# Optimization experiments

Hardware: AMD Instinct MI355X
Metric: run time of the kernel (lower is better)

Reference implementation:

```python
import jax, jax.numpy as jnp
import numpy as np

RADIUS = 0.1
NSAMPLE = 32
B, N, NPOINT, C = 2, 16384, 4096, 64


def setup_inputs() -> dict:
    key = jax.random.key(0)
    k1, k2, k3 = jax.random.split(key, 3)
    xyz = jax.random.uniform(k1, (B, N, 3), dtype=jnp.float32)
    new_xyz = jax.random.uniform(k2, (B, NPOINT, 3), dtype=jnp.float32)
    features = jax.random.normal(k3, (B, C, N), dtype=jnp.float32)
    return {"xyz": xyz, "new_xyz": new_xyz, "features": features}


def ball_query(radius, nsample, xyz, new_xyz):
    # xyz: (B, N, 3), new_xyz: (B, npoint, 3) -> idx: (B, npoint, nsample) int32
    # Semantics of the CUDA ball_query: take the first `nsample` points (in
    # original order) whose squared distance < radius^2; pad remaining slots
    # with the first in-ball index (0 if the ball is empty).
    d2 = jnp.sum((new_xyz[:, :, None, :] - xyz[:, None, :, :]) ** 2, axis=-1)  # (B, npoint, N)
    mask = d2 < radius * radius
    # stable argsort puts in-ball indices first, preserving original order
    order = jnp.argsort(jnp.where(mask, 0, 1), axis=-1)  # (B, npoint, N)
    cnt = jnp.sum(mask, axis=-1, keepdims=True)  # (B, npoint, 1)
    first = jnp.where(cnt > 0, order[..., :1], 0)  # (B, npoint, 1)
    slots = jnp.arange(nsample)
    idx = jnp.where(slots < cnt, order[..., :nsample], first)
    return idx.astype(jnp.int32)


def group(features, idx):
    # features: (B, C, N), idx: (B, npoint, nsample) -> (B, C, npoint, nsample)
    return jax.vmap(lambda f, i: f[:, i])(features, idx)


def reference(xyz, new_xyz, features):
    idx = ball_query(RADIUS, NSAMPLE, xyz, new_xyz)  # (B, npoint, nsample)
    xyz_t = jnp.transpose(xyz, (0, 2, 1))  # (B, 3, N)
    grouped_xyz = group(xyz_t, idx)  # (B, 3, npoint, nsample)
    grouped_xyz = grouped_xyz - jnp.transpose(new_xyz, (0, 2, 1))[..., None]
    grouped_features = group(features, idx)  # (B, C, npoint, nsample)
    new_features = jnp.concatenate([grouped_xyz, grouped_features], axis=1)
    return new_features  # (B, 3 + C, npoint, nsample)
```

## Files before the change

### kernel.cpp

```cpp
#include <hip/hip_runtime.h>

#define B 2
#define N 16384
#define NPOINT 4096
#define C 64
#define NSAMPLE 32

#define NCELL 1000
#define CELLW_STRIDE 1024
#define OFF_STRIDE 1056
#define CAP 192

__device__ __forceinline__ float r2_thresh() { return (float)(0.1 * 0.1); }

__device__ __forceinline__ int clamp09(int v) { return v < 0 ? 0 : (v > 9 ? 9 : v); }

__device__ __forceinline__ int cell_of(float x, float y, float z) {
    const int ix = clamp09((int)floorf(x * 10.0f));
    const int iy = clamp09((int)floorf(y * 10.0f));
    const int iz = clamp09((int)floorf(z * 10.0f));
    return (ix * 10 + iy) * 10 + iz;
}

__global__ void __launch_bounds__(256) grid_init_kernel(int* __restrict__ work) {
    const int t = blockIdx.x * blockDim.x + threadIdx.x;
    if (t < 2 * B * CELLW_STRIDE) work[t] = 0;
}

__global__ void __launch_bounds__(256) grid_hist_kernel(
    const float* __restrict__ xyz, const float* __restrict__ new_xyz,
    int* __restrict__ cellwork, int* __restrict__ qwork) {
    const int i = blockIdx.x * blockDim.x + threadIdx.x;
    if (i < B * N) {
        const int b = i / N;
        const float x = xyz[(size_t)i * 3 + 0];
        const float y = xyz[(size_t)i * 3 + 1];
        const float z = xyz[(size_t)i * 3 + 2];
        atomicAdd(&cellwork[b * CELLW_STRIDE + cell_of(x, y, z)], 1);
    } else if (i < B * (N + NPOINT)) {
        const int qi = i - B * N;
        const int b = qi / NPOINT;
        const float x = new_xyz[(size_t)qi * 3 + 0];
        const float y = new_xyz[(size_t)qi * 3 + 1];
        const float z = new_xyz[(size_t)qi * 3 + 2];
        atomicAdd(&qwork[b * CELLW_STRIDE + cell_of(x, y, z)], 1);
    }
}

__global__ void __launch_bounds__(1024) grid_scan_kernel(
    int* __restrict__ cellwork, int* __restrict__ qwork, int* __restrict__ off) {
    __shared__ int s[1024];
    const int blk = blockIdx.x;
    const int t = threadIdx.x;
    int* __restrict__ arr = (blk < B) ? (cellwork + blk * CELLW_STRIDE)
                                      : (qwork + (blk - B) * CELLW_STRIDE);
    const int v = (t < NCELL) ? arr[t] : 0;
    s[t] = v;
    __syncthreads();
#pragma unroll
    for (int d = 1; d < 1024; d <<= 1) {
        const int add = (t >= d) ? s[t - d] : 0;
        __syncthreads();
        s[t] += add;
        __syncthreads();
    }
    const int excl = s[t] - v;
    if (blk < B && t <= NCELL) off[blk * OFF_STRIDE + t] = excl;
    if (t < NCELL) arr[t] = excl;
}

__global__ void __launch_bounds__(256) grid_scatter_kernel(
    const float* __restrict__ xyz, const float* __restrict__ new_xyz,
    int* __restrict__ cellwork, int* __restrict__ qwork,
    float4* __restrict__ binned, int* __restrict__ qperm) {
    const int i = blockIdx.x * blockDim.x + threadIdx.x;
    if (i < B * N) {
        const int b = i / N;
        const int p = i - b * N;
        const float x = xyz[(size_t)i * 3 + 0];
        const float y = xyz[(size_t)i * 3 + 1];
        const float z = xyz[(size_t)i * 3 + 2];
        const int c = cell_of(x, y, z);
        const int pos = atomicAdd(&cellwork[b * CELLW_STRIDE + c], 1);
        float4 v;
        v.x = x; v.y = y; v.z = z; v.w = __int_as_float(p);
        binned[(size_t)b * N + pos] = v;
    } else if (i < B * (N + NPOINT)) {
        const int qi = i - B * N;
        const int b = qi / NPOINT;
        const int j = qi - b * NPOINT;
        const float x = new_xyz[(size_t)qi * 3 + 0];
        const float y = new_xyz[(size_t)qi * 3 + 1];
        const float z = new_xyz[(size_t)qi * 3 + 2];
        const int c = cell_of(x, y, z);
        const int pos = atomicAdd(&qwork[b * CELLW_STRIDE + c], 1);
        qperm[b * NPOINT + pos] = j;
    }
}

__device__ void linear_ball_fallback(const float* __restrict__ xb,
                                     float cx, float cy, float cz,
                                     int lane, unsigned long long lanemask_lt,
                                     int* __restrict__ out) {
    const float r2 = r2_thresh();
    int cnt = 0, first_idx = 0;
    for (int base = 0; base < N; base += 64) {
        const int i = base + lane;
        const float x = xb[i * 3 + 0];
        const float y = xb[i * 3 + 1];
        const float z = xb[i * 3 + 2];
        float d2;
        {
#pragma clang fp contract(off)
            float dx = x - cx;
            float dy = y - cy;
            float dz = z - cz;
            d2 = dx * dx + dy * dy + dz * dz;
        }
        const bool in = d2 < r2;
        const unsigned long long m = __ballot(in);
        if (in) {
            const int pos = cnt + __popcll(m & lanemask_lt);
            if (pos < NSAMPLE) out[pos] = i;
        }
        if (cnt == 0 && m != 0ull) first_idx = base + __builtin_ctzll(m);
        cnt += __popcll(m);
        if (cnt >= NSAMPLE) break;
    }
    if (cnt < NSAMPLE) {
        if (cnt == 0) first_idx = 0;
        for (int pos = cnt + lane; pos < NSAMPLE; pos += 64) out[pos] = first_idx;
    }
}

__global__ void __launch_bounds__(256) ball_query_grid_kernel(
    const float4* __restrict__ binned,
    const int* __restrict__ off,
    const float* __restrict__ new_xyz,
    const float* __restrict__ xyz,
    const int* __restrict__ qperm,
    int* __restrict__ idx_out)
{
    __shared__ int cand_s[4][CAP];
    const int lane = threadIdx.x & 63;
    const int wib = threadIdx.x >> 6;
    const int wave = (blockIdx.x * blockDim.x + threadIdx.x) >> 6;
    if (wave >= B * NPOINT) return;
    const int b = wave / NPOINT;
    const int sp = wave - b * NPOINT;
    const int j = qperm[b * NPOINT + sp];

    const float cx = new_xyz[((size_t)b * NPOINT + j) * 3 + 0];
    const float cy = new_xyz[((size_t)b * NPOINT + j) * 3 + 1];
    const float cz = new_xyz[((size_t)b * NPOINT + j) * 3 + 2];

    int* __restrict__ cand = cand_s[wib];
    const float4* __restrict__ bb = binned + (size_t)b * N;
    const int* __restrict__ ob = off + b * OFF_STRIDE;
    int* __restrict__ out = idx_out + ((size_t)b * NPOINT + j) * NSAMPLE;

    const float r2 = r2_thresh();
    const unsigned long long lanemask_lt = (lane == 63) ? 0x7FFFFFFFFFFFFFFFull
                                                        : ((1ull << lane) - 1ull);

    const int lox = max(0, (int)floorf((cx - 0.1001f) * 10.0f));
    const int hix = min(9, (int)floorf((cx + 0.1001f) * 10.0f));
    const int loy = max(0, (int)floorf((cy - 0.1001f) * 10.0f));
    const int hiy = min(9, (int)floorf((cy + 0.1001f) * 10.0f));
    const int loz = max(0, (int)floorf((cz - 0.1001f) * 10.0f));
    const int hiz = min(9, (int)floorf((cz + 0.1001f) * 10.0f));

    int K = 0;
    for (int ix = lox; ix <= hix; ++ix) {
        for (int iy = loy; iy <= hiy; ++iy) {
            const int rowc = (ix * 10 + iy) * 10;
            const int s0 = ob[rowc + loz];
            const int s1 = ob[rowc + hiz + 1];
            for (int cur = s0; cur < s1; cur += 64) {
                const int i = cur + lane;
                const bool valid = (i < s1);
                float4 pv;
                if (valid) pv = bb[i];
                else { pv.x = 1e9f; pv.y = 1e9f; pv.z = 1e9f; pv.w = 0.0f; }
                float d2;
                {
#pragma clang fp contract(off)
                    float dx = pv.x - cx;
                    float dy = pv.y - cy;
                    float dz = pv.z - cz;
                    d2 = dx * dx + dy * dy + dz * dz;
                }
                const bool in = valid && (d2 < r2);
                const unsigned long long m = __ballot(in);
                if (in) {
                    const int pos = K + __popcll(m & lanemask_lt);
                    if (pos < CAP) cand[pos] = __float_as_int(pv.w);
                }
                K += __popcll(m);
            }
        }
    }

    if (K > CAP) {
        linear_ball_fallback(xyz + (size_t)b * N * 3, cx, cy, cz, lane, lanemask_lt, out);
        return;
    }

    const int e0 = (lane < K) ? cand[lane] : 0x7FFFFFFF;
    const int e1 = (64 + lane < K) ? cand[64 + lane] : 0x7FFFFFFF;
    const int e2 = (128 + lane < K) ? cand[128 + lane] : 0x7FFFFFFF;
    int r0 = 0, r1 = 0, r2i = 0;
    if (K <= 64) {
        for (int k = 0; k < K; ++k) { const int v = cand[k]; r0 += (v < e0); }
    } else if (K <= 128) {
        for (int k = 0; k < K; ++k) { const int v = cand[k]; r0 += (v < e0); r1 += (v < e1); }
    } else {
        for (int k = 0; k < K; ++k) {
            const int v = cand[k];
            r0 += (v < e0); r1 += (v < e1); r2i += (v < e2);
        }
    }
    if (lane < K && r0 < NSAMPLE) out[r0] = e0;
    if (64 + lane < K && r1 < NSAMPLE) out[r1] = e1;
    if (128 + lane < K && r2i < NSAMPLE) out[r2i] = e2;

    if (K < NSAMPLE) {
        int mn = min(e0, min(e1, e2));
#pragma unroll
        for (int d = 32; d; d >>= 1) mn = min(mn, __shfl_xor(mn, d));
        const int fill = (K > 0) ? mn : 0;
        for (int pos = K + lane; pos < NSAMPLE; pos += 64) out[pos] = fill;
    }
}

__global__ void __launch_bounds__(256) ball_query_kernel(
    const float* __restrict__ xyz, const float* __restrict__ new_xyz,
    int* __restrict__ idx_out)
{
    const int wave = (blockIdx.x * blockDim.x + threadIdx.x) >> 6;
    const int lane = threadIdx.x & 63;
    if (wave >= B * NPOINT) return;
    const int b = wave / NPOINT;
    const float cx = new_xyz[(size_t)wave * 3 + 0];
    const float cy = new_xyz[(size_t)wave * 3 + 1];
    const float cz = new_xyz[(size_t)wave * 3 + 2];
    const unsigned long long lanemask_lt = (lane == 63) ? 0x7FFFFFFFFFFFFFFFull
                                                        : ((1ull << lane) - 1ull);
    linear_ball_fallback(xyz + (size_t)b * N * 3, cx, cy, cz, lane, lanemask_lt,
                         idx_out + (size_t)wave * NSAMPLE);
}

__global__ void __launch_bounds__(256) transpose_kernel(
    const float* __restrict__ feat, float* __restrict__ ft) {
    __shared__ float tile[64 * 65];
    const int b = blockIdx.y;
    const int n0 = blockIdx.x * 64;
    const int t = threadIdx.x;
    const int l = t & 63;
    const int w = t >> 6;
#pragma unroll
    for (int it = 0; it < 16; ++it) {
        const int c = it * 4 + w;
        tile[c * 65 + l] = feat[((size_t)b * C + c) * N + n0 + l];
    }
    __syncthreads();
#pragma unroll
    for (int it = 0; it < 16; ++it) {
        const int nn = it * 4 + w;
        ft[((size_t)b * N + n0 + nn) * C + l] = tile[l * 65 + nn];
    }
}

__global__ void __launch_bounds__(256) group2_kernel(
    const float* __restrict__ xyz, const float* __restrict__ new_xyz,
    const float* __restrict__ ft, const int* __restrict__ idx_arr,
    const int* __restrict__ qperm, float* __restrict__ out) {
    __shared__ int sidx[64];
    __shared__ float sf[64 * 65];

    const int t = threadIdx.x;
    const int g = blockIdx.x;
    const int nwg = B * NPOINT / 2;
    const int swz = (g & 7) * (nwg / 8) + (g >> 3);
    const int b = swz / (NPOINT / 2);
    const int p = swz - b * (NPOINT / 2);

    const int q0 = qperm[b * NPOINT + 2 * p + 0];
    const int q1 = qperm[b * NPOINT + 2 * p + 1];

    if (t < 64) {
        const int qq = (t < 32) ? q0 : q1;
        sidx[t] = idx_arr[((size_t)b * NPOINT + qq) * NSAMPLE + (t & 31)];
    }
    __syncthreads();

    {
        const int lane16 = t & 15;
        const int pq = t >> 4;
#pragma unroll
        for (int it = 0; it < 4; ++it) {
            const int pp = it * 16 + pq;
            const int id = sidx[pp];
            const float4 v = *(const float4*)(ft + ((size_t)b * N + id) * C + lane16 * 4);
            float* dst = sf + pp * 65 + lane16 * 4;
            dst[0] = v.x; dst[1] = v.y; dst[2] = v.z; dst[3] = v.w;
        }
    }

    const size_t plane = (size_t)NPOINT * NSAMPLE;
    const size_t bbase = (size_t)b * (3 + C) * plane;

    if (t < 64) {
        const int id = sidx[t];
        const int qq = (t < 32) ? q0 : q1;
        const size_t cb = ((size_t)b * NPOINT + qq) * 3;
        const size_t pb = ((size_t)b * N + id) * 3;
        const size_t ob = bbase + (size_t)qq * NSAMPLE + (t & 31);
        {
#pragma clang fp contract(off)
            out[ob + 0 * plane] = xyz[pb + 0] - new_xyz[cb + 0];
            out[ob + 1 * plane] = xyz[pb + 1] - new_xyz[cb + 1];
            out[ob + 2 * plane] = xyz[pb + 2] - new_xyz[cb + 2];
        }
    }
    __syncthreads();

    const int l = t & 63;
    const int w = t >> 6;
    const int qq = (l < 32) ? q0 : q1;
    const size_t rowbase = bbase + (size_t)qq * NSAMPLE + (l & 31);
#pragma unroll
    for (int it = 0; it < 16; ++it) {
        const int c = it * 4 + w;
        out[rowbase + (size_t)(3 + c) * plane] = sf[l * 65 + c];
    }
}

__global__ void __launch_bounds__(256) group_kernel(
    const float* __restrict__ xyz, const float* __restrict__ new_xyz,
    const float* __restrict__ feat, const int* __restrict__ idx_arr,
    float* __restrict__ out) {
    const int t = threadIdx.x;
    const int s = t & 31;
    const int jl = t >> 5;
    const int j = blockIdx.x * 8 + jl;
    const int b = blockIdx.y;

    const int id = idx_arr[((size_t)b * NPOINT + j) * NSAMPLE + s];

    const float px = xyz[((size_t)b * N + id) * 3 + 0] - new_xyz[((size_t)b * NPOINT + j) * 3 + 0];
    const float py = xyz[((size_t)b * N + id) * 3 + 1] - new_xyz[((size_t)b * NPOINT + j) * 3 + 1];
    const float pz = xyz[((size_t)b * N + id) * 3 + 2] - new_xyz[((size_t)b * NPOINT + j) * 3 + 2];

    const size_t plane = (size_t)NPOINT * NSAMPLE;
    const size_t obase = (size_t)b * (3 + C) * plane + (size_t)j * NSAMPLE + s;

    out[obase + 0 * plane] = px;
    out[obase + 1 * plane] = py;
    out[obase + 2 * plane] = pz;

    const float* __restrict__ fb = feat + (size_t)b * C * N;
#pragma unroll 8
    for (int c = 0; c < C; ++c) {
        out[obase + (size_t)(3 + c) * plane] = fb[(size_t)c * N + id];
    }
}

extern "C" void kernel_launch(void* const* d_in, const int* in_sizes, int n_in,
                              void* d_out, int out_size, void* d_ws, size_t ws_size,
                              hipStream_t stream) {
    const float* xyz     = (const float*)d_in[0];
    const float* new_xyz = (const float*)d_in[1];
    const float* feat    = (const float*)d_in[2];
    float* out = (float*)d_out;

    const size_t idx_bytes    = (size_t)B * NPOINT * NSAMPLE * sizeof(int);
    const size_t ft_bytes     = (size_t)B * N * C * sizeof(float);
    const size_t binned_bytes = (size_t)B * N * sizeof(float4);
    const size_t off_bytes    = (size_t)B * OFF_STRIDE * sizeof(int);
    const size_t cellw_bytes  = (size_t)B * CELLW_STRIDE * sizeof(int);
    const size_t qwork_bytes  = (size_t)B * CELLW_STRIDE * sizeof(int);
    const size_t qperm_bytes  = (size_t)B * NPOINT * sizeof(int);

    char* ws = (char*)d_ws;
    size_t o = 0;
    int*    idx_ws   = (int*)(ws + o);    o += idx_bytes;
    float*  ft       = (float*)(ws + o);  o += ft_bytes;
    float4* binned   = (float4*)(ws + o); o += binned_bytes;
    int*    off      = (int*)(ws + o);    o += off_bytes;
    int*    cellwork = (int*)(ws + o);    o += cellw_bytes;
    int*    qwork    = (int*)(ws + o);    o += qwork_bytes;
    int*    qperm    = (int*)(ws + o);    o += qperm_bytes;

    const bool use_grid = (ws_size >= o);

    if (use_grid) {
        transpose_kernel<<<dim3(N / 64, B), 256, 0, stream>>>(feat, ft);
        grid_init_kernel<<<(2 * B * CELLW_STRIDE + 255) / 256, 256, 0, stream>>>(cellwork);
        grid_hist_kernel<<<(B * (N + NPOINT) + 255) / 256, 256, 0, stream>>>(
            xyz, new_xyz, cellwork, qwork);
        grid_scan_kernel<<<2 * B, 1024, 0, stream>>>(cellwork, qwork, off);
        grid_scatter_kernel<<<(B * (N + NPOINT) + 255) / 256, 256, 0, stream>>>(
            xyz, new_xyz, cellwork, qwork, binned, qperm);
        ball_query_grid_kernel<<<(B * NPOINT) / 4, 256, 0, stream>>>(
            binned, off, new_xyz, xyz, qperm, idx_ws);
        group2_kernel<<<B * NPOINT / 2, 256, 0, stream>>>(
            xyz, new_xyz, ft, idx_ws, qperm, out);
    } else {
        ball_query_kernel<<<(B * NPOINT) / 4, 256, 0, stream>>>(xyz, new_xyz, idx_ws);
        dim3 grid2(NPOINT / 8, B);
        group_kernel<<<grid2, 256, 0, stream>>>(xyz, new_xyz, feat, idx_ws, out);
    }
}
```

Baseline: 54.48 us.

## Process two cell-sorted queries per wave sharing candidate scans when windows match

After: 56.65 us. 4.0% more time.

```diff
diff --git a/kernel.cpp b/kernel.cpp
--- a/kernel.cpp
+++ b/kernel.cpp
@@ -101,7 +101,7 @@
 __device__ void linear_ball_fallback(const float* __restrict__ xb,
                                      float cx, float cy, float cz,
                                      int lane, unsigned long long lanemask_lt,
-                                     int* __restrict__ out) {
+                                     int* out) {
     const float r2 = r2_thresh();
     int cnt = 0, first_idx = 0;
     for (int base = 0; base < N; base += 64) {
@@ -133,43 +133,42 @@
     }
 }
 
-__global__ void __launch_bounds__(256) ball_query_grid_kernel(
-    const float4* __restrict__ binned,
-    const int* __restrict__ off,
-    const float* __restrict__ new_xyz,
-    const float* __restrict__ xyz,
-    const int* __restrict__ qperm,
-    int* __restrict__ idx_out)
+__device__ __forceinline__ void rank_select(const int* cand, int K, int lane,
+                                            int* __restrict__ out) {
+    const int e0 = (lane < K) ? cand[lane] : 0x7FFFFFFF;
+    const int e1 = (64 + lane < K) ? cand[64 + lane] : 0x7FFFFFFF;
+    const int e2 = (128 + lane < K) ? cand[128 + lane] : 0x7FFFFFFF;
+    int r0 = 0, r1 = 0, r2i = 0;
+    if (K <= 64) {
+        for (int k = 0; k < K; ++k) { const int v = cand[k]; r0 += (v < e0); }
+    } else if (K <= 128) {
+        for (int k = 0; k < K; ++k) { const int v = cand[k]; r0 += (v < e0); r1 += (v < e1); }
+    } else {
+        for (int k = 0; k < K; ++k) {
+            const int v = cand[k];
+            r0 += (v < e0); r1 += (v < e1); r2i += (v < e2);
+        }
+    }
+    if (lane < K && r0 < NSAMPLE) out[r0] = e0;
+    if (64 + lane < K && r1 < NSAMPLE) out[r1] = e1;
+    if (128 + lane < K && r2i < NSAMPLE) out[r2i] = e2;
+
+    if (K < NSAMPLE) {
+        int mn = min(e0, min(e1, e2));
+#pragma unroll
+        for (int d = 32; d; d >>= 1) mn = min(mn, __shfl_xor(mn, d));
+        const int fill = (K > 0) ? mn : 0;
+        for (int pos = K + lane; pos < NSAMPLE; pos += 64) out[pos] = fill;
+    }
+}
+
+__device__ __forceinline__ int scan_window(
+    const float4* __restrict__ bb, const int* __restrict__ ob,
+    int lox, int hix, int loy, int hiy, int loz, int hiz,
+    float cx, float cy, float cz, int lane,
+    unsigned long long lanemask_lt, int* cand)
 {
-    __shared__ int cand_s[4][CAP];
-    const int lane = threadIdx.x & 63;
-    const int wib = threadIdx.x >> 6;
-    const int wave = (blockIdx.x * blockDim.x + threadIdx.x) >> 6;
-    if (wave >= B * NPOINT) return;
-    const int b = wave / NPOINT;
-    const int sp = wave - b * NPOINT;
-    const int j = qperm[b * NPOINT + sp];
-
-    const float cx = new_xyz[((size_t)b * NPOINT + j) * 3 + 0];
-    const float cy = new_xyz[((size_t)b * NPOINT + j) * 3 + 1];
-    const float cz = new_xyz[((size_t)b * NPOINT + j) * 3 + 2];
-
-    int* __restrict__ cand = cand_s[wib];
-    const float4* __restrict__ bb = binned + (size_t)b * N;
-    const int* __restrict__ ob = off + b * OFF_STRIDE;
-    int* __restrict__ out = idx_out + ((size_t)b * NPOINT + j) * NSAMPLE;
-
     const float r2 = r2_thresh();
-    const unsigned long long lanemask_lt = (lane == 63) ? 0x7FFFFFFFFFFFFFFFull
-                                                        : ((1ull << lane) - 1ull);
-
-    const int lox = max(0, (int)floorf((cx - 0.1001f) * 10.0f));
-    const int hix = min(9, (int)floorf((cx + 0.1001f) * 10.0f));
-    const int loy = max(0, (int)floorf((cy - 0.1001f) * 10.0f));
-    const int hiy = min(9, (int)floorf((cy + 0.1001f) * 10.0f));
-    const int loz = max(0, (int)floorf((cz - 0.1001f) * 10.0f));
-    const int hiz = min(9, (int)floorf((cz + 0.1001f) * 10.0f));
-
     int K = 0;
     for (int ix = lox; ix <= hix; ++ix) {
         for (int iy = loy; iy <= hiy; ++iy) {
@@ -185,9 +184,7 @@
                 float d2;
                 {
 #pragma clang fp contract(off)
-                    float dx = pv.x - cx;
-                    float dy = pv.y - cy;
-                    float dz = pv.z - cz;
+                    float dx = pv.x - cx, dy = pv.y - cy, dz = pv.z - cz;
                     d2 = dx * dx + dy * dy + dz * dz;
                 }
                 const bool in = valid && (d2 < r2);
@@ -200,36 +197,207 @@
             }
         }
     }
-
-    if (K > CAP) {
-        linear_ball_fallback(xyz + (size_t)b * N * 3, cx, cy, cz, lane, lanemask_lt, out);
-        return;
-    }
-
-    const int e0 = (lane < K) ? cand[lane] : 0x7FFFFFFF;
-    const int e1 = (64 + lane < K) ? cand[64 + lane] : 0x7FFFFFFF;
-    const int e2 = (128 + lane < K) ? cand[128 + lane] : 0x7FFFFFFF;
-    int r0 = 0, r1 = 0, r2i = 0;
-    if (K <= 64) {
-        for (int k = 0; k < K; ++k) { const int v = cand[k]; r0 += (v < e0); }
-    } else if (K <= 128) {
-        for (int k = 0; k < K; ++k) { const int v = cand[k]; r0 += (v < e0); r1 += (v < e1); }
+    return K;
+}
+
+__global__ void __launch_bounds__(256) ball_query_pair_kernel(
+    const float4* __restrict__ binned,
+    const int* __restrict__ off,
+    const float* __restrict__ new_xyz,
+    const float* __restrict__ xyz,
+    const int* __restrict__ qperm,
+    int* __restrict__ idx_out)
+{
+    __shared__ int cand_s[8][CAP];
+    const int lane = threadIdx.x & 63;
+    const int wib = threadIdx.x >> 6;
+
+    const int nwg = B * NPOINT / 8;
+    const int g = blockIdx.x;
+    const int swz = (g & 7) * (nwg / 8) + (g >> 3);
+    const int gw = swz * 4 + wib;
+    const int b = gw / (NPOINT / 2);
+    const int r = gw % (NPOINT / 2);
+
+    const int j0 = qperm[b * NPOINT + 2 * r + 0];
+    const int j1 = qperm[b * NPOINT + 2 * r + 1];
+
+    const float c0x = new_xyz[((size_t)b * NPOINT + j0) * 3 + 0];
+    const float c0y = new_xyz[((size_t)b * NPOINT + j0) * 3 + 1];
+    const float c0z = new_xyz[((size_t)b * NPOINT + j0) * 3 + 2];
+    const float c1x = new_xyz[((size_t)b * NPOINT + j1) * 3 + 0];
+    const float c1y = new_xyz[((size_t)b * NPOINT + j1) * 3 + 1];
+    const float c1z = new_xyz[((size_t)b * NPOINT + j1) * 3 + 2];
+
+    int* cand0 = cand_s[wib * 2 + 0];
+    int* cand1 = cand_s[wib * 2 + 1];
+    const float4* __restrict__ bb = binned + (size_t)b * N;
+    const int* __restrict__ ob = off + b * OFF_STRIDE;
+    int* __restrict__ out0 = idx_out + ((size_t)b * NPOINT + j0) * NSAMPLE;
+    int* __restrict__ out1 = idx_out + ((size_t)b * NPOINT + j1) * NSAMPLE;
+
+    const float r2 = r2_thresh();
+    const unsigned long long lanemask_lt = (lane == 63) ? 0x7FFFFFFFFFFFFFFFull
+                                                        : ((1ull << lane) - 1ull);
+
+    const int l0x = max(0, (int)floorf((c0x - 0.1001f) * 10.0f));
+    const int h0x = min(9, (int)floorf((c0x + 0.1001f) * 10.0f));
+    const int l0y = max(0, (int)floorf((c0y - 0.1001f) * 10.0f));
+    const int h0y = min(9, (int)floorf((c0y + 0.1001f) * 10.0f));
+    const int l0z = max(0, (int)floorf((c0z - 0.1001f) * 10.0f));
+    const int h0z = min(9, (int)floorf((c0z + 0.1001f) * 10.0f));
+    const int l1x = max(0, (int)floorf((c1x - 0.1001f) * 10.0f));
+    const int h1x = min(9, (int)floorf((c1x + 0.1001f) * 10.0f));
+    const int l1y = max(0, (int)floorf((c1y - 0.1001f) * 10.0f));
+    const int h1y = min(9, (int)floorf((c1y + 0.1001f) * 10.0f));
+    const int l1z = max(0, (int)floorf((c1z - 0.1001f) * 10.0f));
+    const int h1z = min(9, (int)floorf((c1z + 0.1001f) * 10.0f));
+
+    const bool same_window = (l0x == l1x) && (h0x == h1x) &&
+                             (l0y == l1y) && (h0y == h1y) &&
+                             (l0z == l1z) && (h0z == h1z);
+
+    int K0 = 0, K1 = 0;
+    if (same_window) {
+        for (int ix = l0x; ix <= h0x; ++ix) {
+            for (int iy = l0y; iy <= h0y; ++iy) {
+                const int rowc = (ix * 10 + iy) * 10;
+                const int s0 = ob[rowc + l0z];
+                const int s1 = ob[rowc + h0z + 1];
+                for (int cur = s0; cur < s1; cur += 64) {
+                    const int i = cur + lane;
+                    const bool valid = (i < s1);
+                    float4 pv;
+                    if (valid) pv = bb[i];
+                    else { pv.x = 1e9f; pv.y = 1e9f; pv.z = 1e9f; pv.w = 0.0f; }
+                    float d20, d21;
+                    {
+#pragma clang fp contract(off)
+                        float dx0 = pv.x - c0x, dy0 = pv.y - c0y, dz0 = pv.z - c0z;
+                        d20 = dx0 * dx0 + dy0 * dy0 + dz0 * dz0;
+                        float dx1 = pv.x - c1x, dy1 = pv.y - c1y, dz1 = pv.z - c1z;
+                        d21 = dx1 * dx1 + dy1 * dy1 + dz1 * dz1;
+                    }
+                    const bool in0 = valid && (d20 < r2);
+                    const bool in1 = valid && (d21 < r2);
+                    const unsigned long long m0 = __ballot(in0);
+                    const unsigned long long m1 = __ballot(in1);
+                    const int id = __float_as_int(pv.w);
+                    if (in0) {
+                        const int pos = K0 + __popcll(m0 & lanemask_lt);
+                        if (pos < CAP) cand0[pos] = id;
+                    }
+                    if (in1) {
+                        const int pos = K1 + __popcll(m1 & lanemask_lt);
+                        if (pos < CAP) cand1[pos] = id;
+                    }
+                    K0 += __popcll(m0);
+                    K1 += __popcll(m1);
+                }
+            }
+        }
     } else {
-        for (int k = 0; k < K; ++k) {
-            const int v = cand[k];
-            r0 += (v < e0); r1 += (v < e1); r2i += (v < e2);
-        }
-    }
-    if (lane < K && r0 < NSAMPLE) out[r0] = e0;
-    if (64 + lane < K && r1 < NSAMPLE) out[r1] = e1;
-    if (128 + lane < K && r2i < NSAMPLE) out[r2i] = e2;
-
-    if (K < NSAMPLE) {
-        int mn = min(e0, min(e1, e2));
-#pragma unroll
-        for (int d = 32; d; d >>= 1) mn = min(mn, __shfl_xor(mn, d));
-        const int fill = (K > 0) ? mn : 0;
-        for (int pos = K + lane; pos < NSAMPLE; pos += 64) out[pos] = fill;
+        K0 = scan_window(bb, ob, l0x, h0x, l0y, h0y, l0z, h0z,
+                         c0x, c0y, c0z, lane, lanemask_lt, cand0);
+        K1 = scan_window(bb, ob, l1x, h1x, l1y, h1y, l1z, h1z,
+                         c1x, c1y, c1z, lane, lanemask_lt, cand1);
+    }
+
+    if (K0 > CAP) {
+        linear_ball_fallback(xyz + (size_t)b * N * 3, c0x, c0y, c0z, lane, lanemask_lt, out0);
+    } else {
+        rank_select(cand0, K0, lane, out0);
+    }
+    if (K1 > CAP) {
+        linear_ball_fallback(xyz + (size_t)b * N * 3, c1x, c1y, c1z, lane, lanemask_lt, out1);
+    } else {
+        rank_select(cand1, K1, lane, out1);
+    }
+}
+
+__global__ void __launch_bounds__(256) transpose_kernel(
+    const float* __restrict__ feat, float* __restrict__ ft) {
+    __shared__ float tile[64 * 65];
+    const int b = blockIdx.y;
+    const int n0 = blockIdx.x * 64;
+    const int t = threadIdx.x;
+    const int l = t & 63;
+    const int w = t >> 6;
+#pragma unroll
+    for (int it = 0; it < 16; ++it) {
+        const int c = it * 4 + w;
+        tile[c * 65 + l] = feat[((size_t)b * C + c) * N + n0 + l];
+    }
+    __syncthreads();
+#pragma unroll
+    for (int it = 0; it < 16; ++it) {
+        const int nn = it * 4 + w;
+        ft[((size_t)b * N + n0 + nn) * C + l] = tile[l * 65 + nn];
+    }
+}
+
+__global__ void __launch_bounds__(256) group2_kernel(
+    const float* __restrict__ xyz, const float* __restrict__ new_xyz,
+    const float* __restrict__ ft, const int* __restrict__ idx_arr,
+    const int* __restrict__ qperm, float* __restrict__ out) {
+    __shared__ int sidx[64];
+    __shared__ float sf[64 * 65];
+
+    const int t = threadIdx.x;
+    const int g = blockIdx.x;
+    const int nwg = B * NPOINT / 2;
+    const int swz = (g & 7) * (nwg / 8) + (g >> 3);
+    const int b = swz / (NPOINT / 2);
+    const int p = swz - b * (NPOINT / 2);
+
+    const int q0 = qperm[b * NPOINT + 2 * p + 0];
+    const int q1 = qperm[b * NPOINT + 2 * p + 1];
+
+    if (t < 64) {
+        const int qq = (t < 32) ? q0 : q1;
+        sidx[t] = idx_arr[((size_t)b * NPOINT + qq) * NSAMPLE + (t & 31)];
+    }
+    __syncthreads();
+
+    {
+        const int lane16 = t & 15;
+        const int pq = t >> 4;
+#pragma unroll
+        for (int it = 0; it < 4; ++it) {
+            const int pp = it * 16 + pq;
+            const int id = sidx[pp];
+            const float4 v = *(const float4*)(ft + ((size_t)b * N + id) * C + lane16 * 4);
+            float* dst = sf + pp * 65 + lane16 * 4;
+            dst[0] = v.x; dst[1] = v.y; dst[2] = v.z; dst[3] = v.w;
+        }
+    }
+
+    const size_t plane = (size_t)NPOINT * NSAMPLE;
+    const size_t bbase = (size_t)b * (3 + C) * plane;
+
+    if (t < 64) {
+        const int id = sidx[t];
+        const int qq = (t < 32) ? q0 : q1;
+        const size_t cb = ((size_t)b * NPOINT + qq) * 3;
+        const size_t pb = ((size_t)b * N + id) * 3;
+        const size_t ob = bbase + (size_t)qq * NSAMPLE + (t & 31);
+        {
+#pragma clang fp contract(off)
+            out[ob + 0 * plane] = xyz[pb + 0] - new_xyz[cb + 0];
+            out[ob + 1 * plane] = xyz[pb + 1] - new_xyz[cb + 1];
+            out[ob + 2 * plane] = xyz[pb + 2] - new_xyz[cb + 2];
+        }
+    }
+    __syncthreads();
+
+    const int l = t & 63;
+    const int w = t >> 6;
+    const int qq = (l < 32) ? q0 : q1;
+    const size_t rowbase = bbase + (size_t)qq * NSAMPLE + (l & 31);
+#pragma unroll
+    for (int it = 0; it < 16; ++it) {
+        const int c = it * 4 + w;
+        out[rowbase + (size_t)(3 + c) * plane] = sf[l * 65 + c];
     }
 }
 
@@ -250,92 +418,6 @@
                          idx_out + (size_t)wave * NSAMPLE);
 }
 
-__global__ void __launch_bounds__(256) transpose_kernel(
-    const float* __restrict__ feat, float* __restrict__ ft) {
-    __shared__ float tile[64 * 65];
-    const int b = blockIdx.y;
-    const int n0 = blockIdx.x * 64;
-    const int t = threadIdx.x;
-    const int l = t & 63;
-    const int w = t >> 6;
-#pragma unroll
-    for (int it = 0; it < 16; ++it) {
-        const int c = it * 4 + w;
-        tile[c * 65 + l] = feat[((size_t)b * C + c) * N + n0 + l];
-    }
-    __syncthreads();
-#pragma unroll
-    for (int it = 0; it < 16; ++it) {
-        const int nn = it * 4 + w;
-        ft[((size_t)b * N + n0 + nn) * C + l] = tile[l * 65 + nn];
-    }
-}
-
-__global__ void __launch_bounds__(256) group2_kernel(
-    const float* __restrict__ xyz, const float* __restrict__ new_xyz,
-    const float* __restrict__ ft, const int* __restrict__ idx_arr,
-    const int* __restrict__ qperm, float* __restrict__ out) {
-    __shared__ int sidx[64];
-    __shared__ float sf[64 * 65];
-
-    const int t = threadIdx.x;
-    const int g = blockIdx.x;
-    const int nwg = B * NPOINT / 2;
-    const int swz = (g & 7) * (nwg / 8) + (g >> 3);
-    const int b = swz / (NPOINT / 2);
-    const int p = swz - b * (NPOINT / 2);
-
-    const int q0 = qperm[b * NPOINT + 2 * p + 0];
-    const int q1 = qperm[b * NPOINT + 2 * p + 1];
-
-    if (t < 64) {
-        const int qq = (t < 32) ? q0 : q1;
-        sidx[t] = idx_arr[((size_t)b * NPOINT + qq) * NSAMPLE + (t & 31)];
-    }
-    __syncthreads();
-
-    {
-        const int lane16 = t & 15;
-        const int pq = t >> 4;
-#pragma unroll
-        for (int it = 0; it < 4; ++it) {
-            const int pp = it * 16 + pq;
-            const int id = sidx[pp];
-            const float4 v = *(const float4*)(ft + ((size_t)b * N + id) * C + lane16 * 4);
-            float* dst = sf + pp * 65 + lane16 * 4;
-            dst[0] = v.x; dst[1] = v.y; dst[2] = v.z; dst[3] = v.w;
-        }
-    }
-
-    const size_t plane = (size_t)NPOINT * NSAMPLE;
-    const size_t bbase = (size_t)b * (3 + C) * plane;
-
-    if (t < 64) {
-        const int id = sidx[t];
-        const int qq = (t < 32) ? q0 : q1;
-        const size_t cb = ((size_t)b * NPOINT + qq) * 3;
-        const size_t pb = ((size_t)b * N + id) * 3;
-        const size_t ob = bbase + (size_t)qq * NSAMPLE + (t & 31);
-        {
-#pragma clang fp contract(off)
-            out[ob + 0 * plane] = xyz[pb + 0] - new_xyz[cb + 0];
-            out[ob + 1 * plane] = xyz[pb + 1] - new_xyz[cb + 1];
-            out[ob + 2 * plane] = xyz[pb + 2] - new_xyz[cb + 2];
-        }
-    }
-    __syncthreads();
-
-    const int l = t & 63;
-    const int w = t >> 6;
-    const int qq = (l < 32) ? q0 : q1;
-    const size_t rowbase = bbase + (size_t)qq * NSAMPLE + (l & 31);
-#pragma unroll
-    for (int it = 0; it < 16; ++it) {
-        const int c = it * 4 + w;
-        out[rowbase + (size_t)(3 + c) * plane] = sf[l * 65 + c];
-    }
-}
-
 __global__ void __launch_bounds__(256) group_kernel(
     const float* __restrict__ xyz, const float* __restrict__ new_xyz,
     const float* __restrict__ feat, const int* __restrict__ idx_arr,
@@ -402,7 +484,7 @@
         grid_scan_kernel<<<2 * B, 1024, 0, stream>>>(cellwork, qwork, off);
         grid_scatter_kernel<<<(B * (N + NPOINT) + 255) / 256, 256, 0, stream>>>(
             xyz, new_xyz, cellwork, qwork, binned, qperm);
-        ball_query_grid_kernel<<<(B * NPOINT) / 4, 256, 0, stream>>>(
+        ball_query_pair_kernel<<<B * NPOINT / 8, 256, 0, stream>>>(
             binned, off, new_xyz, xyz, qperm, idx_ws);
         group2_kernel<<<B * NPOINT / 2, 256, 0, stream>>>(
             xyz, new_xyz, ft, idx_ws, qperm, out);
```

## Merge feature transpose into ball-query launch, use wave-shuffle scan, memset init

Applied to the files above, without the earlier changes.

New measurement: 52.55 us. -3.6%, faster.

```diff
diff --git a/kernel.cpp b/kernel.cpp
--- a/kernel.cpp
+++ b/kernel.cpp
@@ -11,6 +11,9 @@
 #define OFF_STRIDE 1056
 #define CAP 192
 
+#define BALL_BLOCKS (B * NPOINT / 4)
+#define TRANS_BLOCKS (B * (N / 64))
+
 __device__ __forceinline__ float r2_thresh() { return (float)(0.1 * 0.1); }
 
 __device__ __forceinline__ int clamp09(int v) { return v < 0 ? 0 : (v > 9 ? 9 : v); }
@@ -20,11 +23,6 @@
     const int iy = clamp09((int)floorf(y * 10.0f));
     const int iz = clamp09((int)floorf(z * 10.0f));
     return (ix * 10 + iy) * 10 + iz;
-}
-
-__global__ void __launch_bounds__(256) grid_init_kernel(int* __restrict__ work) {
-    const int t = blockIdx.x * blockDim.x + threadIdx.x;
-    if (t < 2 * B * CELLW_STRIDE) work[t] = 0;
 }
 
 __global__ void __launch_bounds__(256) grid_hist_kernel(
@@ -49,22 +47,35 @@
 
 __global__ void __launch_bounds__(1024) grid_scan_kernel(
     int* __restrict__ cellwork, int* __restrict__ qwork, int* __restrict__ off) {
-    __shared__ int s[1024];
+    __shared__ int wsum[16];
     const int blk = blockIdx.x;
     const int t = threadIdx.x;
+    const int lane = t & 63;
+    const int w = t >> 6;
     int* __restrict__ arr = (blk < B) ? (cellwork + blk * CELLW_STRIDE)
                                       : (qwork + (blk - B) * CELLW_STRIDE);
     const int v = (t < NCELL) ? arr[t] : 0;
-    s[t] = v;
+
+    int s = v;
+#pragma unroll
+    for (int d = 1; d < 64; d <<= 1) {
+        const int u = __shfl_up(s, d, 64);
+        if (lane >= d) s += u;
+    }
+    if (lane == 63) wsum[w] = s;
     __syncthreads();
-#pragma unroll
-    for (int d = 1; d < 1024; d <<= 1) {
-        const int add = (t >= d) ? s[t - d] : 0;
-        __syncthreads();
-        s[t] += add;
-        __syncthreads();
-    }
-    const int excl = s[t] - v;
+    if (w == 0) {
+        int p = (lane < 16) ? wsum[lane] : 0;
+#pragma unroll
+        for (int d = 1; d < 16; d <<= 1) {
+            const int u = __shfl_up(p, d, 64);
+            if (lane >= d) p += u;
+        }
+        if (lane < 16) wsum[lane] = p;
+    }
+    __syncthreads();
+    const int prefix = (w > 0) ? wsum[w - 1] : 0;
+    const int excl = s + prefix - v;
     if (blk < B && t <= NCELL) off[blk * OFF_STRIDE + t] = excl;
     if (t < NCELL) arr[t] = excl;
 }
@@ -101,7 +112,7 @@
 __device__ void linear_ball_fallback(const float* __restrict__ xb,
                                      float cx, float cy, float cz,
                                      int lane, unsigned long long lanemask_lt,
-                                     int* __restrict__ out) {
+                                     int* out) {
     const float r2 = r2_thresh();
     int cnt = 0, first_idx = 0;
     for (int base = 0; base < N; base += 64) {
@@ -133,43 +144,42 @@
     }
 }
 
-__global__ void __launch_bounds__(256) ball_query_grid_kernel(
-    const float4* __restrict__ binned,
-    const int* __restrict__ off,
-    const float* __restrict__ new_xyz,
-    const float* __restrict__ xyz,
-    const int* __restrict__ qperm,
-    int* __restrict__ idx_out)
+__device__ __forceinline__ void rank_select(const int* cand, int K, int lane,
+                                            int* __restrict__ out) {
+    const int e0 = (lane < K) ? cand[lane] : 0x7FFFFFFF;
+    const int e1 = (64 + lane < K) ? cand[64 + lane] : 0x7FFFFFFF;
+    const int e2 = (128 + lane < K) ? cand[128 + lane] : 0x7FFFFFFF;
+    int r0 = 0, r1 = 0, r2i = 0;
+    if (K <= 64) {
+        for (int k = 0; k < K; ++k) { const int v = cand[k]; r0 += (v < e0); }
+    } else if (K <= 128) {
+        for (int k = 0; k < K; ++k) { const int v = cand[k]; r0 += (v < e0); r1 += (v < e1); }
+    } else {
+        for (int k = 0; k < K; ++k) {
+            const int v = cand[k];
+            r0 += (v < e0); r1 += (v < e1); r2i += (v < e2);
+        }
+    }
+    if (lane < K && r0 < NSAMPLE) out[r0] = e0;
+    if (64 + lane < K && r1 < NSAMPLE) out[r1] = e1;
+    if (128 + lane < K && r2i < NSAMPLE) out[r2i] = e2;
+
+    if (K < NSAMPLE) {
+        int mn = min(e0, min(e1, e2));
+#pragma unroll
+        for (int d = 32; d; d >>= 1) mn = min(mn, __shfl_xor(mn, d));
+        const int fill = (K > 0) ? mn : 0;
+        for (int pos = K + lane; pos < NSAMPLE; pos += 64) out[pos] = fill;
+    }
+}
+
+__device__ __forceinline__ int scan_window(
+    const float4* __restrict__ bb, const int* __restrict__ ob,
+    int lox, int hix, int loy, int hiy, int loz, int hiz,
+    float cx, float cy, float cz, int lane,
+    unsigned long long lanemask_lt, int* cand)
 {
-    __shared__ int cand_s[4][CAP];
-    const int lane = threadIdx.x & 63;
-    const int wib = threadIdx.x >> 6;
-    const int wave = (blockIdx.x * blockDim.x + threadIdx.x) >> 6;
-    if (wave >= B * NPOINT) return;
-    const int b = wave / NPOINT;
-    const int sp = wave - b * NPOINT;
-    const int j = qperm[b * NPOINT + sp];
-
-    const float cx = new_xyz[((size_t)b * NPOINT + j) * 3 + 0];
-    const float cy = new_xyz[((size_t)b * NPOINT + j) * 3 + 1];
-    const float cz = new_xyz[((size_t)b * NPOINT + j) * 3 + 2];
-
-    int* __restrict__ cand = cand_s[wib];
-    const float4* __restrict__ bb = binned + (size_t)b * N;
-    const int* __restrict__ ob = off + b * OFF_STRIDE;
-    int* __restrict__ out = idx_out + ((size_t)b * NPOINT + j) * NSAMPLE;
-
     const float r2 = r2_thresh();
-    const unsigned long long lanemask_lt = (lane == 63) ? 0x7FFFFFFFFFFFFFFFull
-                                                        : ((1ull << lane) - 1ull);
-
-    const int lox = max(0, (int)floorf((cx - 0.1001f) * 10.0f));
-    const int hix = min(9, (int)floorf((cx + 0.1001f) * 10.0f));
-    const int loy = max(0, (int)floorf((cy - 0.1001f) * 10.0f));
-    const int hiy = min(9, (int)floorf((cy + 0.1001f) * 10.0f));
-    const int loz = max(0, (int)floorf((cz - 0.1001f) * 10.0f));
-    const int hiz = min(9, (int)floorf((cz + 0.1001f) * 10.0f));
-
     int K = 0;
     for (int ix = lox; ix <= hix; ++ix) {
         for (int iy = loy; iy <= hiy; ++iy) {
@@ -185,9 +195,7 @@
                 float d2;
                 {
 #pragma clang fp contract(off)
-                    float dx = pv.x - cx;
-                    float dy = pv.y - cy;
-                    float dz = pv.z - cz;
+                    float dx = pv.x - cx, dy = pv.y - cy, dz = pv.z - cz;
                     d2 = dx * dx + dy * dy + dz * dz;
                 }
                 const bool in = valid && (d2 < r2);
@@ -200,36 +208,142 @@
             }
         }
     }
+    return K;
+}
+
+__global__ void __launch_bounds__(256) ball_and_transpose_kernel(
+    const float4* __restrict__ binned,
+    const int* __restrict__ off,
+    const float* __restrict__ new_xyz,
+    const float* __restrict__ xyz,
+    const int* __restrict__ qperm,
+    int* __restrict__ idx_out,
+    const float* __restrict__ feat,
+    float* __restrict__ ft)
+{
+    __shared__ int cand_s[4][CAP];
+    __shared__ float tile[64 * 65];
+
+    const int t = threadIdx.x;
+
+    if (blockIdx.x >= BALL_BLOCKS) {
+        const int tb = blockIdx.x - BALL_BLOCKS;
+        const int b = tb / (N / 64);
+        const int n0 = (tb % (N / 64)) * 64;
+        const int l = t & 63;
+        const int w = t >> 6;
+#pragma unroll
+        for (int it = 0; it < 16; ++it) {
+            const int c = it * 4 + w;
+            tile[c * 65 + l] = feat[((size_t)b * C + c) * N + n0 + l];
+        }
+        __syncthreads();
+#pragma unroll
+        for (int it = 0; it < 16; ++it) {
+            const int nn = it * 4 + w;
+            ft[((size_t)b * N + n0 + nn) * C + l] = tile[l * 65 + nn];
+        }
+        return;
+    }
+
+    const int lane = t & 63;
+    const int wib = t >> 6;
+    const int wave = blockIdx.x * 4 + wib;
+    const int b = wave / NPOINT;
+    const int sp = wave - b * NPOINT;
+    const int j = qperm[b * NPOINT + sp];
+
+    const float cx = new_xyz[((size_t)b * NPOINT + j) * 3 + 0];
+    const float cy = new_xyz[((size_t)b * NPOINT + j) * 3 + 1];
+    const float cz = new_xyz[((size_t)b * NPOINT + j) * 3 + 2];
+
+    int* cand = cand_s[wib];
+    const float4* __restrict__ bb = binned + (size_t)b * N;
+    const int* __restrict__ ob = off + b * OFF_STRIDE;
+    int* __restrict__ out = idx_out + ((size_t)b * NPOINT + j) * NSAMPLE;
+
+    const unsigned long long lanemask_lt = (lane == 63) ? 0x7FFFFFFFFFFFFFFFull
+                                                        : ((1ull << lane) - 1ull);
+
+    const int lox = max(0, (int)floorf((cx - 0.1001f) * 10.0f));
+    const int hix = min(9, (int)floorf((cx + 0.1001f) * 10.0f));
+    const int loy = max(0, (int)floorf((cy - 0.1001f) * 10.0f));
+    const int hiy = min(9, (int)floorf((cy + 0.1001f) * 10.0f));
+    const int loz = max(0, (int)floorf((cz - 0.1001f) * 10.0f));
+    const int hiz = min(9, (int)floorf((cz + 0.1001f) * 10.0f));
+
+    const int K = scan_window(bb, ob, lox, hix, loy, hiy, loz, hiz,
+                              cx, cy, cz, lane, lanemask_lt, cand);
 
     if (K > CAP) {
         linear_ball_fallback(xyz + (size_t)b * N * 3, cx, cy, cz, lane, lanemask_lt, out);
-        return;
-    }
-
-    const int e0 = (lane < K) ? cand[lane] : 0x7FFFFFFF;
-    const int e1 = (64 + lane < K) ? cand[64 + lane] : 0x7FFFFFFF;
-    const int e2 = (128 + lane < K) ? cand[128 + lane] : 0x7FFFFFFF;
-    int r0 = 0, r1 = 0, r2i = 0;
-    if (K <= 64) {
-        for (int k = 0; k < K; ++k) { const int v = cand[k]; r0 += (v < e0); }
-    } else if (K <= 128) {
-        for (int k = 0; k < K; ++k) { const int v = cand[k]; r0 += (v < e0); r1 += (v < e1); }
     } else {
-        for (int k = 0; k < K; ++k) {
-            const int v = cand[k];
-            r0 += (v < e0); r1 += (v < e1); r2i += (v < e2);
-        }
-    }
-    if (lane < K && r0 < NSAMPLE) out[r0] = e0;
-    if (64 + lane < K && r1 < NSAMPLE) out[r1] = e1;
-    if (128 + lane < K && r2i < NSAMPLE) out[r2i] = e2;
-
-    if (K < NSAMPLE) {
-        int mn = min(e0, min(e1, e2));
-#pragma unroll
-        for (int d = 32; d; d >>= 1) mn = min(mn, __shfl_xor(mn, d));
-        const int fill = (K > 0) ? mn : 0;
-        for (int pos = K + lane; pos < NSAMPLE; pos += 64) out[pos] = fill;
+        rank_select(cand, K, lane, out);
+    }
+}
+
+__global__ void __launch_bounds__(256) group2_kernel(
+    const float* __restrict__ xyz, const float* __restrict__ new_xyz,
+    const float* __restrict__ ft, const int* __restrict__ idx_arr,
+    const int* __restrict__ qperm, float* __restrict__ out) {
+    __shared__ int sidx[64];
+    __shared__ float sf[64 * 65];
+
+    const int t = threadIdx.x;
+    const int g = blockIdx.x;
+    const int nwg = B * NPOINT / 2;
+    const int swz = (g & 7) * (nwg / 8) + (g >> 3);
+    const int b = swz / (NPOINT / 2);
+    const int p = swz - b * (NPOINT / 2);
+
+    const int q0 = qperm[b * NPOINT + 2 * p + 0];
+    const int q1 = qperm[b * NPOINT + 2 * p + 1];
+
+    if (t < 64) {
+        const int qq = (t < 32) ? q0 : q1;
+        sidx[t] = idx_arr[((size_t)b * NPOINT + qq) * NSAMPLE + (t & 31)];
+    }
+    __syncthreads();
+
+    {
+        const int lane16 = t & 15;
+        const int pq = t >> 4;
+#pragma unroll
+        for (int it = 0; it < 4; ++it) {
+            const int pp = it * 16 + pq;
+            const int id = sidx[pp];
+            const float4 v = *(const float4*)(ft + ((size_t)b * N + id) * C + lane16 * 4);
+            float* dst = sf + pp * 65 + lane16 * 4;
+            dst[0] = v.x; dst[1] = v.y; dst[2] = v.z; dst[3] = v.w;
+        }
+    }
+
+    const size_t plane = (size_t)NPOINT * NSAMPLE;
+    const size_t bbase = (size_t)b * (3 + C) * plane;
+
+    if (t < 64) {
+        const int id = sidx[t];
+        const int qq = (t < 32) ? q0 : q1;
+        const size_t cb = ((size_t)b * NPOINT + qq) * 3;
+        const size_t pb = ((size_t)b * N + id) * 3;
+        const size_t ob = bbase + (size_t)qq * NSAMPLE + (t & 31);
+        {
+#pragma clang fp contract(off)
+            out[ob + 0 * plane] = xyz[pb + 0] - new_xyz[cb + 0];
+            out[ob + 1 * plane] = xyz[pb + 1] - new_xyz[cb + 1];
+            out[ob + 2 * plane] = xyz[pb + 2] - new_xyz[cb + 2];
+        }
+    }
+    __syncthreads();
+
+    const int l = t & 63;
+    const int w = t >> 6;
+    const int qq = (l < 32) ? q0 : q1;
+    const size_t rowbase = bbase + (size_t)qq * NSAMPLE + (l & 31);
+#pragma unroll
+    for (int it = 0; it < 16; ++it) {
+        const int c = it * 4 + w;
+        out[rowbase + (size_t)(3 + c) * plane] = sf[l * 65 + c];
     }
 }
 
@@ -250,92 +364,6 @@
                          idx_out + (size_t)wave * NSAMPLE);
 }
 
-__global__ void __launch_bounds__(256) transpose_kernel(
-    const float* __restrict__ feat, float* __restrict__ ft) {
-    __shared__ float tile[64 * 65];
-    const int b = blockIdx.y;
-    const int n0 = blockIdx.x * 64;
-    const int t = threadIdx.x;
-    const int l = t & 63;
-    const int w = t >> 6;
-#pragma unroll
-    for (int it = 0; it < 16; ++it) {
-        const int c = it * 4 + w;
-        tile[c * 65 + l] = feat[((size_t)b * C + c) * N + n0 + l];
-    }
-    __syncthreads();
-#pragma unroll
-    for (int it = 0; it < 16; ++it) {
-        const int nn = it * 4 + w;
-        ft[((size_t)b * N + n0 + nn) * C + l] = tile[l * 65 + nn];
-    }
-}
-
-__global__ void __launch_bounds__(256) group2_kernel(
-    const float* __restrict__ xyz, const float* __restrict__ new_xyz,
-    const float* __restrict__ ft, const int* __restrict__ idx_arr,
-    const int* __restrict__ qperm, float* __restrict__ out) {
-    __shared__ int sidx[64];
-    __shared__ float sf[64 * 65];
-
-    const int t = threadIdx.x;
-    const int g = blockIdx.x;
-    const int nwg = B * NPOINT / 2;
-    const int swz = (g & 7) * (nwg / 8) + (g >> 3);
-    const int b = swz / (NPOINT / 2);
-    const int p = swz - b * (NPOINT / 2);
-
-    const int q0 = qperm[b * NPOINT + 2 * p + 0];
-    const int q1 = qperm[b * NPOINT + 2 * p + 1];
-
-    if (t < 64) {
-        const int qq = (t < 32) ? q0 : q1;
-        sidx[t] = idx_arr[((size_t)b * NPOINT + qq) * NSAMPLE + (t & 31)];
-    }
-    __syncthreads();
-
-    {
-        const int lane16 = t & 15;
-        const int pq = t >> 4;
-#pragma unroll
-        for (int it = 0; it < 4; ++it) {
-            const int pp = it * 16 + pq;
-            const int id = sidx[pp];
-            const float4 v = *(const float4*)(ft + ((size_t)b * N + id) * C + lane16 * 4);
-            float* dst = sf + pp * 65 + lane16 * 4;
-            dst[0] = v.x; dst[1] = v.y; dst[2] = v.z; dst[3] = v.w;
-        }
-    }
-
-    const size_t plane = (size_t)NPOINT * NSAMPLE;
-    const size_t bbase = (size_t)b * (3 + C) * plane;
-
-    if (t < 64) {
-        const int id = sidx[t];
-        const int qq = (t < 32) ? q0 : q1;
-        const size_t cb = ((size_t)b * NPOINT + qq) * 3;
-        const size_t pb = ((size_t)b * N + id) * 3;
-        const size_t ob = bbase + (size_t)qq * NSAMPLE + (t & 31);
-        {
-#pragma clang fp contract(off)
-            out[ob + 0 * plane] = xyz[pb + 0] - new_xyz[cb + 0];
-            out[ob + 1 * plane] = xyz[pb + 1] - new_xyz[cb + 1];
-            out[ob + 2 * plane] = xyz[pb + 2] - new_xyz[cb + 2];
-        }
-    }
-    __syncthreads();
-
-    const int l = t & 63;
-    const int w = t >> 6;
-    const int qq = (l < 32) ? q0 : q1;
-    const size_t rowbase = bbase + (size_t)qq * NSAMPLE + (l & 31);
-#pragma unroll
-    for (int it = 0; it < 16; ++it) {
-        const int c = it * 4 + w;
-        out[rowbase + (size_t)(3 + c) * plane] = sf[l * 65 + c];
-    }
-}
-
 __global__ void __launch_bounds__(256) group_kernel(
     const float* __restrict__ xyz, const float* __restrict__ new_xyz,
     const float* __restrict__ feat, const int* __restrict__ idx_arr,
@@ -395,15 +423,14 @@
     const bool use_grid = (ws_size >= o);
 
     if (use_grid) {
-        transpose_kernel<<<dim3(N / 64, B), 256, 0, stream>>>(feat, ft);
-        grid_init_kernel<<<(2 * B * CELLW_STRIDE + 255) / 256, 256, 0, stream>>>(cellwork);
+        hipMemsetAsync(cellwork, 0, cellw_bytes + qwork_bytes, stream);
         grid_hist_kernel<<<(B * (N + NPOINT) + 255) / 256, 256, 0, stream>>>(
             xyz, new_xyz, cellwork, qwork);
         grid_scan_kernel<<<2 * B, 1024, 0, stream>>>(cellwork, qwork, off);
         grid_scatter_kernel<<<(B * (N + NPOINT) + 255) / 256, 256, 0, stream>>>(
             xyz, new_xyz, cellwork, qwork, binned, qperm);
-        ball_query_grid_kernel<<<(B * NPOINT) / 4, 256, 0, stream>>>(
-            binned, off, new_xyz, xyz, qperm, idx_ws);
+        ball_and_transpose_kernel<<<BALL_BLOCKS + TRANS_BLOCKS, 256, 0, stream>>>(
+            binned, off, new_xyz, xyz, qperm, idx_ws, feat, ft);
         group2_kernel<<<B * NPOINT / 2, 256, 0, stream>>>(
             xyz, new_xyz, ft, idx_ws, qperm, out);
     } else {
```
